# Performance work log

Measured on AMD Instinct MI355X. Metric: run time of the kernel, lower is better.

The kernel has to match this reference:

```python
import jax, jax.numpy as jnp
import numpy as np

B, S, TK, H, E, V, OOV = 16, 8, 400, 256, 128, 50000, 50
H2 = 2 * H


def setup_inputs() -> dict:
    key = jax.random.key(0)
    ks = jax.random.split(key, 24)
    std = 0.02
    d = {}
    d["y_t_1"] = jax.random.randint(ks[0], (B,), 0, V)
    d["h0"] = jax.random.normal(ks[1], (B, H), jnp.float32)
    d["c0"] = jax.random.normal(ks[2], (B, H), jnp.float32)
    d["encoder_output"] = jax.random.normal(ks[3], (B, S, TK, H2), jnp.float32)
    d["section_output"] = jax.random.normal(ks[4], (B, S, H2), jnp.float32)
    d["enc_padding_mask"] = jnp.ones((B, S, TK), jnp.float32)
    d["c_t_1"] = jax.random.normal(ks[5], (B, H2), jnp.float32)
    d["extra_zeros"] = jnp.zeros((B, OOV), jnp.float32)
    d["enc_batch_extend_vocab"] = jax.random.randint(ks[6], (B, S * TK), 0, V + OOV)
    d["coverage"] = jnp.zeros((B, S, TK), jnp.float32)
    d["gamma"] = jnp.ones((B, S, TK), jnp.float32)
    # learned parameters
    d["embedding"] = std * jax.random.normal(ks[7], (V, E), jnp.float32)
    d["W_xc"] = std * jax.random.normal(ks[8], (H2 + E, E), jnp.float32)
    d["b_xc"] = jnp.zeros((E,), jnp.float32)
    d["W_ih"] = std * jax.random.normal(ks[9], (E, 4 * H), jnp.float32)
    d["b_ih"] = jnp.zeros((4 * H,), jnp.float32)
    d["W_hh"] = std * jax.random.normal(ks[10], (H, 4 * H), jnp.float32)
    # pytorch init sets forget-gate bias (2nd quarter) to 1
    d["b_hh"] = jnp.zeros((4 * H,), jnp.float32).at[H:2 * H].set(1.0)
    d["Wh_sec"] = std * jax.random.normal(ks[11], (H2, H2), jnp.float32)
    d["Wd_sec"] = std * jax.random.normal(ks[12], (H2, H2), jnp.float32)
    d["bd_sec"] = jnp.zeros((H2,), jnp.float32)
    d["v_sec"] = std * jax.random.normal(ks[13], (H2, 1), jnp.float32)
    d["Wh_w"] = std * jax.random.normal(ks[14], (H2, H2), jnp.float32)
    d["Wc_w"] = std * jax.random.normal(ks[15], (H2,), jnp.float32)
    d["Wd_w"] = std * jax.random.normal(ks[16], (H2, H2), jnp.float32)
    d["bd_w"] = jnp.zeros((H2,), jnp.float32)
    d["v_w"] = std * jax.random.normal(ks[17], (H2, 1), jnp.float32)
    d["W_pgen"] = std * jax.random.normal(ks[18], (4 * H + E, 1), jnp.float32)
    d["b_pgen"] = jnp.zeros((1,), jnp.float32)
    d["W_out1"] = std * jax.random.normal(ks[19], (3 * H, H), jnp.float32)
    d["b_out1"] = jnp.zeros((H,), jnp.float32)
    d["W_out2"] = std * jax.random.normal(ks[20], (H, V), jnp.float32)
    d["b_out2"] = jnp.zeros((V,), jnp.float32)
    return d


def reference(y_t_1, h0, c0, encoder_output, section_output, enc_padding_mask,
              c_t_1, extra_zeros, enc_batch_extend_vocab, coverage, gamma,
              embedding, W_xc, b_xc, W_ih, b_ih, W_hh, b_hh,
              Wh_sec, Wd_sec, bd_sec, v_sec,
              Wh_w, Wc_w, Wd_w, bd_w, v_w,
              W_pgen, b_pgen, W_out1, b_out1, W_out2, b_out2):
    # embedding + input context projection
    emb = embedding[y_t_1]                                      # [B,E]
    x = jnp.concatenate([c_t_1, emb], axis=1) @ W_xc + b_xc     # [B,E]
    # single-step LSTM (pytorch gate order i,f,g,o)
    gates = x @ W_ih + b_ih + h0 @ W_hh + b_hh                  # [B,4H]
    i, f, g, o = jnp.split(gates, 4, axis=1)
    c = jax.nn.sigmoid(f) * c0 + jax.nn.sigmoid(i) * jnp.tanh(g)
    h = jax.nn.sigmoid(o) * jnp.tanh(c)
    s_t_hat = jnp.concatenate([h, c], axis=1)                   # [B,2H]
    # section attention -> beta [B,S]
    e_sec = jnp.tanh(section_output @ Wh_sec + (s_t_hat @ Wd_sec + bd_sec)[:, None, :])
    sc_sec = jnp.squeeze(e_sec @ v_sec, -1)                     # [B,S]
    beta = jax.nn.softmax(sc_sec, axis=1)
    beta = beta / beta.sum(axis=1, keepdims=True)
    # word attention with coverage feature
    att = encoder_output @ Wh_w + (s_t_hat @ Wd_w + bd_w)[:, None, None, :]
    att = att + coverage[..., None] * Wc_w                      # [B,S,TK,2H]
    sc_w = jnp.squeeze(jnp.tanh(att) @ v_w, -1)                 # [B,S,TK]
    ws = (beta[:, :, None] * sc_w).reshape(B, S * TK)
    mask = enc_padding_mask.reshape(B, S * TK)
    ad = jax.nn.softmax(ws, axis=1) * mask
    attn = ad / ad.sum(axis=1, keepdims=True)                   # [B,S*TK]
    c_t = jnp.einsum('bt,btn->bn', attn, encoder_output.reshape(B, S * TK, H2))
    cov = coverage + attn.reshape(B, S, TK)
    # pointer-gen gate
    p_gen = jax.nn.sigmoid(jnp.concatenate([c_t, s_t_hat, x], axis=1) @ W_pgen + b_pgen)  # [B,1]
    # output vocab distribution
    out = jnp.concatenate([h, c_t], axis=1) @ W_out1 + b_out1
    vocab_dist = jax.nn.softmax(out @ W_out2 + b_out2, axis=1)  # [B,V]
    vd = jnp.concatenate([p_gen * vocab_dist, extra_zeros], axis=1)  # [B,V+OOV]
    ad_ = (1.0 - p_gen) * attn
    rows = jnp.arange(B)[:, None]
    final_dist = vd.at[rows, enc_batch_extend_vocab].add(ad_)
    return (final_dist, h, c, c_t, attn, p_gen, cov)
```

## Files before the change

kernel.cpp:

```cpp
#include <hip/hip_runtime.h>
#include <math.h>

#define BB   16
#define SS   8
#define TKK  400
#define HH   256
#define EE   128
#define VV   50000
#define OOVV 50
#define HH2  512
#define STK  (SS*TKK)
#define VOO  (VV+OOVV)

#define OFF_X     0
#define OFF_ST    2048
#define OFF_SD    10240
#define OFF_WD    18432
#define OFF_SCSEC 26752
#define OFF_SCW   26880
#define OFF_CT    78080
#define OFF_OUT1  86272
#define OFF_PGEN  90368
#define OFF_PSUM  93520
#define OFF_ASUM  99776
#define OFF_BT    113040

#define O_FD   0
#define O_H    800800
#define O_C    804896
#define O_CT   808992
#define O_ATTN 817184
#define O_PGEN 868384
#define O_COV  868400

#define NLB 391
#define GEMM_NB 800

typedef __attribute__((ext_vector_type(8))) short bf16x8;
typedef __attribute__((ext_vector_type(4))) float f32x4;

__device__ __forceinline__ float sigm(float x){ return 1.0f/(1.0f+expf(-x)); }

__device__ __forceinline__ unsigned short f2b(float f){
  unsigned int u = __float_as_uint(f);
  unsigned int r = (u + 0x7fffu + ((u >> 16) & 1u)) >> 16;
  return (unsigned short)r;
}

__device__ __forceinline__ float tanhfast(float x){
  float cx = fminf(9.0f, fmaxf(-9.0f, x));
  float t = __expf(2.0f*cx);
  return (t - 1.0f) * __builtin_amdgcn_rcpf(t + 1.0f);
}

__device__ __forceinline__ float wave_sum(float v){
  #pragma unroll
  for(int o=32;o>0;o>>=1) v += __shfl_xor(v,o);
  return v;
}

__device__ __forceinline__ void glds16(const void* g, void* l){
  __builtin_amdgcn_global_load_lds((const __attribute__((address_space(1))) void*)g,
                                   (__attribute__((address_space(3))) void*)l, 16, 0, 0);
}

__device__ __forceinline__ bf16x8 cvt8(float4 a, float4 b){
  union{ bf16x8 v; unsigned short u[8]; } t;
  t.u[0]=f2b(a.x); t.u[1]=f2b(a.y); t.u[2]=f2b(a.z); t.u[3]=f2b(a.w);
  t.u[4]=f2b(b.x); t.u[5]=f2b(b.y); t.u[6]=f2b(b.z); t.u[7]=f2b(b.w);
  return t.v;
}

__global__ void k_pre(const float* __restrict__ Whw, unsigned short* __restrict__ Btg,
                      const int* __restrict__ y, const float* __restrict__ ct1,
                      const float* __restrict__ emb, const float* __restrict__ Wxc,
                      const float* __restrict__ bxc, const float* __restrict__ bdsec,
                      const float* __restrict__ bdw, float* __restrict__ ws){
  __shared__ float sm[10440];
  int bi = blockIdx.x, tid = threadIdx.x;
  if(bi < 64){
    int n0 = (bi & 7)*64, k0 = (bi >> 3)*64;
    int tx = tid & 63, ty = tid >> 6;
    #pragma unroll
    for(int it=0; it<16; it++){
      int kk = it*4 + ty;
      sm[kk*65 + tx] = Whw[(size_t)(k0+kk)*HH2 + n0 + tx];
    }
    __syncthreads();
    #pragma unroll
    for(int it=0; it<2; it++){
      int kgl = it*4 + ty;
      int kgG = (k0 >> 3) + kgl;
      int rnd = kgG >> 2, kg = kgG & 3;
      int col = n0 + tx;
      union{ bf16x8 v; unsigned short u[8]; } t;
      #pragma unroll
      for(int j=0;j<8;j++) t.u[j] = f2b(sm[(kgl*8+j)*65 + tx]);
      *(bf16x8*)&Btg[(size_t)rnd*16384 + (size_t)(col*4 + (kg ^ ((col>>1)&3)))*8] = t.v;
    }
  } else if(bi < 80){
    float* cat = sm;
    float* red = sm + 10240;
    for(int f=tid; f<BB*640; f+=256){
      int b = f/640, r = f - b*640;
      cat[f] = (r < HH2) ? ct1[b*HH2 + r] : emb[(size_t)y[b]*EE + (r-HH2)];
    }
    __syncthreads();
    int c = (bi-64)*8 + (tid & 7);
    int b = (tid >> 3) & 15;
    int kh = tid >> 7;
    float acc = 0.0f;
    const float* a = &cat[b*640];
    for(int k=kh*320; k<kh*320+320; k++) acc += a[k]*Wxc[k*EE + c];
    if(kh==1) red[b*8 + (tid&7)] = acc;
    __syncthreads();
    if(kh==0) ws[OFF_X + b*EE + c] = acc + red[b*8 + (tid&7)] + bxc[c];
  } else {
    for(int f=tid; f<BB*HH2; f+=256){
      int c = f & (HH2-1);
      ws[OFF_CT + f] = 0.0f;
      ws[OFF_SD + f] = bdsec[c];
      ws[OFF_WD + f] = bdw[c];
    }
    if(tid < BB) ws[OFF_ASUM + tid] = 0.0f;
  }
}

__global__ void k_lstm(const float* __restrict__ h0, const float* __restrict__ c0,
                       const float* __restrict__ Wih, const float* __restrict__ bih,
                       const float* __restrict__ Whh, const float* __restrict__ bhh,
                       float* __restrict__ ws, float* __restrict__ out){
  __shared__ float xh[4*384];
  __shared__ float red[3*64*4];
  int tid = threadIdx.x;
  int jc = (blockIdx.x & 15)*16, bc = (blockIdx.x >> 4)*4;
  for(int f=tid; f<4*384; f+=256){
    int bl = f/384, r = f - bl*384;
    xh[f] = (r < EE) ? ws[OFF_X + (bc+bl)*EE + r] : h0[(bc+bl)*HH + (r-EE)];
  }
  __syncthreads();
  int jl = tid & 15, bl = (tid >> 4) & 3, kq = tid >> 6;
  int j = jc + jl, b = bc + bl;
  float a0=0.f, a1=0.f, a2=0.f, a3=0.f;
  const float* a = &xh[bl*384];
  for(int k=kq*96; k<kq*96+96; k++){
    float v = a[k];
    const float* w = (k < EE) ? &Wih[k*4*HH + j] : &Whh[(k-EE)*4*HH + j];
    a0 += v*w[0]; a1 += v*w[HH]; a2 += v*w[2*HH]; a3 += v*w[3*HH];
  }
  if(kq){
    float* r = &red[((kq-1)*64 + bl*16 + jl)*4];
    r[0]=a0; r[1]=a1; r[2]=a2; r[3]=a3;
  }
  __syncthreads();
  if(kq==0){
    #pragma unroll
    for(int p=0;p<3;p++){
      const float* r = &red[(p*64 + bl*16 + jl)*4];
      a0+=r[0]; a1+=r[1]; a2+=r[2]; a3+=r[3];
    }
    a0 += bih[j] + bhh[j];
    a1 += bih[j+HH] + bhh[j+HH];
    a2 += bih[j+2*HH] + bhh[j+2*HH];
    a3 += bih[j+3*HH] + bhh[j+3*HH];
    float c = sigm(a1)*c0[b*HH+j] + sigm(a0)*tanhf(a2);
    float h = sigm(a3)*tanhf(c);
    out[O_H + b*HH + j] = h;
    out[O_C + b*HH + j] = c;
    ws[OFF_ST + b*HH2 + j]      = h;
    ws[OFF_ST + b*HH2 + HH + j] = c;
  }
}

__global__ void k_proj(const float* __restrict__ Wdsec, const float* __restrict__ Wdw,
                       float* __restrict__ ws){
  __shared__ float st[BB*32];
  int tid = threadIdx.x;
  int mi = blockIdx.x >> 5;
  int cb = (blockIdx.x >> 4) & 1;
  int kq = blockIdx.x & 15;
  int k0 = kq*32;
  for(int f=tid; f<BB*32; f+=256){
    int b = f >> 5, kk = f & 31;
    st[f] = ws[OFF_ST + b*HH2 + k0 + kk];
  }
  __syncthreads();
  int c = cb*256 + tid;
  const float* Wm = (mi ? Wdw : Wdsec) + (size_t)k0*HH2 + c;
  float acc[BB];
  #pragma unroll
  for(int b=0;b<BB;b++) acc[b] = 0.0f;
  #pragma unroll 4
  for(int kk=0;kk<32;kk++){
    float wv = Wm[(size_t)kk*HH2];
    #pragma unroll
    for(int b=0;b<BB;b++) acc[b] += st[b*32 + kk]*wv;
  }
  int dst = mi ? OFF_WD : OFF_SD;
  #pragma unroll
  for(int b=0;b<BB;b++) atomicAdd(&ws[dst + b*HH2 + c], acc[b]);
}

__global__ __launch_bounds__(512, 4) void k_gemm6(
        const float* __restrict__ A, const unsigned short* __restrict__ Btg,
        const float* __restrict__ Wcw, const float* __restrict__ vw,
        const float* __restrict__ cover,
        const float* __restrict__ sec, const float* __restrict__ Whsec,
        const float* __restrict__ vsec, float* __restrict__ ws){
  __shared__ __align__(16) unsigned short smem[32768];
  int tid = threadIdx.x;
  if(blockIdx.x >= GEMM_NB){
    float* row = (float*)smem;
    float* red = row + HH2;
    int bi = blockIdx.x - GEMM_NB;
    int b = bi >> 3;
    if(tid < HH2) row[tid] = sec[(size_t)bi*HH2 + tid];
    __syncthreads();
    int col = tid;
    float acc = 0.0f;
    #pragma unroll 8
    for(int k=0;k<HH2;k++) acc += row[k]*Whsec[k*HH2 + col];
    float val = tanhf(acc + ws[OFF_SD + b*HH2 + col]) * vsec[col];
    val = wave_sum(val);
    if((tid&63)==0) red[tid>>6] = val;
    __syncthreads();
    if(tid==0){
      float s = 0.0f;
      #pragma unroll
      for(int i=0;i<8;i++) s += red[i];
      ws[OFF_SCSEC + bi] = s;
    }
    return;
  }
  int w = tid >> 6, lane = tid & 63, m = lane & 15, q = lane >> 4;
  int mk = (m >> 1) & 3, sw = q ^ mk;
  int rg = w >> 1, cg = w & 1;
  int row0 = blockIdx.x * 64;
  int b = blockIdx.x / 50;

  const float* arow_p = &A[(size_t)(row0 + rg*16 + m)*HH2 + q*8];

  f32x4 acc[16];
  #pragma unroll
  for(int j=0;j<16;j++) acc[j] = (f32x4){0.f,0.f,0.f,0.f};

  #define GLDSB(rr, bufsel) {                                                  \
    const unsigned short* bsrc_ = Btg + (size_t)(rr)*16384;                    \
    _Pragma("unroll")                                                          \
    for(int i_=0;i_<4;i_++)                                                    \
      glds16(bsrc_ + i_*4096 + tid*8, &smem[(bufsel)*16384 + i_*4096 + tid*8]);\
  }

  GLDSB(0, 0);
  float4 pa0 = *(const float4*)(arow_p);
  float4 pa1 = *(const float4*)(arow_p + 4);
  GLDSB(1, 1);
  asm volatile("s_waitcnt vmcnt(6)" ::: "memory");
  __builtin_amdgcn_sched_barrier(0);
  bf16x8 af = cvt8(pa0, pa1);
  __builtin_amdgcn_s_barrier();

  #pragma unroll
  for(int r=0; r<16; r++){
    if(r < 15){
      pa0 = *(const float4*)(arow_p + (r+1)*32);
      pa1 = *(const float4*)(arow_p + (r+1)*32 + 4);
    }
    __builtin_amdgcn_s_setprio(1);
    #pragma unroll
    for(int cf=0; cf<16; cf++){
      int col = cg*256 + cf*16 + m;
      bf16x8 bv = *(const bf16x8*)&smem[(size_t)(r&1)*16384 + ((size_t)col*4 + sw)*8];
      acc[cf] = __builtin_amdgcn_mfma_f32_16x16x32_bf16(af, bv, acc[cf], 0,0,0);
    }
    __builtin_amdgcn_s_setprio(0);
    if(r < 14){
      asm volatile("s_waitcnt lgkmcnt(0)" ::: "memory");
      __builtin_amdgcn_sched_barrier(0);
      __builtin_amdgcn_s_barrier();
      GLDSB(r+2, (r&1));
    }
    if(r < 15){
      if(r < 14){ asm volatile("s_waitcnt vmcnt(6)" ::: "memory"); }
      else      { asm volatile("s_waitcnt vmcnt(2)" ::: "memory"); }
      __builtin_amdgcn_sched_barrier(0);
      af = cvt8(pa0, pa1);
      __builtin_amdgcn_s_barrier();
    }
  }
  #undef GLDSB

  float cov[4];
  #pragma unroll
  for(int r=0;r<4;r++) cov[r] = cover[row0 + rg*16 + q*4 + r];
  float rsum[4] = {0,0,0,0};
  #pragma unroll
  for(int j=0;j<16;j++){
    int col = cg*256 + j*16 + m;
    float wdv = ws[OFF_WD + b*HH2 + col];
    float wcv = Wcw[col], vwv = vw[col];
    #pragma unroll
    for(int r=0;r<4;r++)
      rsum[r] += tanhfast(acc[j][r] + wdv + cov[r]*wcv) * vwv;
  }
  __syncthreads();
  float* rbuf = (float*)smem;
  #pragma unroll
  for(int r=0;r<4;r++){
    float v = rsum[r];
    v += __shfl_xor(v,1,16); v += __shfl_xor(v,2,16);
    v += __shfl_xor(v,4,16); v += __shfl_xor(v,8,16);
    if(m==0) rbuf[cg*64 + rg*16 + q*4 + r] = v;
  }
  __syncthreads();
  if(tid < 64) ws[OFF_SCW + row0 + tid] = rbuf[tid] + rbuf[64 + tid];
}

__global__ void k_attnA(const float* __restrict__ mask, float* __restrict__ ws,
                        float* __restrict__ out){
  int b = blockIdx.y;
  int j = blockIdx.x*256 + threadIdx.x;
  float sc[SS];
  #pragma unroll
  for(int s=0;s<SS;s++) sc[s] = ws[OFF_SCSEC + b*SS + s];
  float bm = -1e30f;
  #pragma unroll
  for(int s=0;s<SS;s++) bm = fmaxf(bm, sc[s]);
  float bsum = 0.0f;
  #pragma unroll
  for(int s=0;s<SS;s++){ sc[s] = expf(sc[s]-bm); bsum += sc[s]; }
  float e = 0.0f;
  if(j < STK){
    float be = sc[j/TKK] / bsum;
    e = expf(be * ws[OFF_SCW + b*STK + j]) * mask[b*STK + j];
    out[O_ATTN + b*STK + j] = e;
  }
  float sv = wave_sum(e);
  if((threadIdx.x & 63) == 0) atomicAdd(&ws[OFF_ASUM + b], sv);
}

__global__ void k_attnB(const float* __restrict__ enc, const float* __restrict__ cover,
                        float* __restrict__ ws, float* __restrict__ out){
  int b = blockIdx.y, tid = threadIdx.x;
  __shared__ float a[64];
  __shared__ float part[512];
  int t0 = blockIdx.x*64;
  float inv = 1.0f / ws[OFF_ASUM + b];
  if(tid < 64){
    float av = out[O_ATTN + b*STK + t0 + tid] * inv;
    a[tid] = av;
    out[O_ATTN + b*STK + t0 + tid] = av;
    out[O_COV  + b*STK + t0 + tid] = cover[b*STK + t0 + tid] + av;
  }
  __syncthreads();
  int c4 = tid & 127, rh = tid >> 7;
  const float4* e4 = (const float4*)enc;
  size_t base = ((size_t)(b*STK + t0 + rh*32))*128 + c4;
  float4 acc = {0.f,0.f,0.f,0.f};
  #pragma unroll 8
  for(int rr=0; rr<32; rr++){
    float4 v = e4[base + (size_t)rr*128];
    float av = a[rh*32 + rr];
    acc.x += av*v.x; acc.y += av*v.y; acc.z += av*v.z; acc.w += av*v.w;
  }
  if(rh) *(float4*)&part[c4*4] = acc;
  __syncthreads();
  if(!rh){
    float4 o = *(const float4*)&part[c4*4];
    atomicAdd(&ws[OFF_CT + b*HH2 + c4*4 + 0], acc.x + o.x);
    atomicAdd(&ws[OFF_CT + b*HH2 + c4*4 + 1], acc.y + o.y);
    atomicAdd(&ws[OFF_CT + b*HH2 + c4*4 + 2], acc.z + o.z);
    atomicAdd(&ws[OFF_CT + b*HH2 + c4*4 + 3], acc.w + o.w);
  }
}

__global__ void k_out1(const float* __restrict__ Wp, const float* __restrict__ bp,
                       const float* __restrict__ Wo1, const float* __restrict__ bo1,
                       float* __restrict__ ws, float* __restrict__ out){
  __shared__ float cat[BB*768];
  __shared__ float red[3*64];
  int tid = threadIdx.x;
  if(blockIdx.x == 64){
    int w = tid >> 6, lane = tid & 63;
    #pragma unroll
    for(int i=0;i<4;i++){
      int b = w*4 + i;
      float p = 0.0f;
      for(int k=lane;k<4*HH+EE;k+=64){
        float val = (k < HH2) ? ws[OFF_CT + b*HH2 + k]
                  : (k < 4*HH) ? ws[OFF_ST + b*HH2 + (k-HH2)]
                  : ws[OFF_X + b*EE + (k-4*HH)];
        p += val * Wp[k];
      }
      p = wave_sum(p);
      if(lane==0){
        float pg = sigm(p + bp[0]);
        ws[OFF_PGEN + b] = pg;
        out[O_PGEN + b]  = pg;
      }
    }
    for(int f=tid; f<BB*HH2; f+=256) out[O_CT + f] = ws[OFF_CT + f];
    return;
  }
  for(int f=tid; f<BB*768; f+=256){
    int b = f/768, r = f - b*768;
    cat[f] = (r < HH) ? ws[OFF_ST + b*HH2 + r] : ws[OFF_CT + b*HH2 + (r-HH)];
  }
  __syncthreads();
  int cl = tid & 3, bl = (tid >> 2) & 15, kq = tid >> 6;
  int c = blockIdx.x*4 + cl;
  float acc = 0.0f;
  const float* a = &cat[bl*768];
  for(int k=kq*192; k<kq*192+192; k++) acc += a[k]*Wo1[k*HH + c];
  if(kq) red[(kq-1)*64 + bl*4 + cl] = acc;
  __syncthreads();
  if(kq==0){
    acc += red[bl*4+cl] + red[64 + bl*4+cl] + red[128 + bl*4+cl];
    ws[OFF_OUT1 + bl*HH + c] = acc + bo1[c];
  }
}

__global__ void k_logits(const float* __restrict__ W2, const float* __restrict__ b2,
                         float* __restrict__ ws, float* __restrict__ out){
  int tid = threadIdx.x;
  __shared__ float o1[BB*HH];
  for(int i=tid;i<BB*HH/4;i+=256)
    ((float4*)o1)[i] = ((const float4*)&ws[OFF_OUT1])[i];
  __syncthreads();
  int cl = tid & 31, bq = tid >> 5;
  int c4 = blockIdx.x*128 + cl*4;
  bool ok = c4 < VV;
  int b0 = bq*2, b1 = b0+1;
  float4 acc0 = {0.f,0.f,0.f,0.f}, acc1 = {0.f,0.f,0.f,0.f};
  if(ok){
    const float* oa = &o1[b0*HH];
    const float* ob = &o1[b1*HH];
    #pragma unroll 4
    for(int k=0;k<HH;k++){
      float4 wv = *(const float4*)&W2[(size_t)k*VV + c4];
      float xa = oa[k], xb = ob[k];
      acc0.x += xa*wv.x; acc0.y += xa*wv.y; acc0.z += xa*wv.z; acc0.w += xa*wv.w;
      acc1.x += xb*wv.x; acc1.y += xb*wv.y; acc1.z += xb*wv.z; acc1.w += xb*wv.w;
    }
  }
  float bv[4] = {0,0,0,0};
  if(ok){ float4 t = *(const float4*)&b2[c4]; bv[0]=t.x; bv[1]=t.y; bv[2]=t.z; bv[3]=t.w; }
  float a0[4] = {acc0.x, acc0.y, acc0.z, acc0.w};
  float a1[4] = {acc1.x, acc1.y, acc1.z, acc1.w};
  float s0 = 0.0f, s1 = 0.0f;
  #pragma unroll
  for(int j=0;j<4;j++){
    float e0 = ok ? expf(a0[j]+bv[j]) : 0.0f;
    float e1 = ok ? expf(a1[j]+bv[j]) : 0.0f;
    if(ok){
      out[(size_t)b0*VOO + c4 + j] = e0;
      out[(size_t)b1*VOO + c4 + j] = e1;
    }
    s0 += e0; s1 += e1;
  }
  #pragma unroll
  for(int o=1;o<32;o<<=1){ s0 += __shfl_xor(s0,o,32); s1 += __shfl_xor(s1,o,32); }
  if(cl==0){
    ws[OFF_PSUM + b0*NLB + blockIdx.x] = s0;
    ws[OFF_PSUM + b1*NLB + blockIdx.x] = s1;
  }
}

__global__ void k_final(const float* __restrict__ xz, float* __restrict__ ws,
                        float* __restrict__ out){
  int b = blockIdx.y;
  int v = blockIdx.x*256 + threadIdx.x;
  __shared__ float red[4];
  int lane = threadIdx.x & 63, w = threadIdx.x >> 6;
  float p = 0.0f;
  for(int i=threadIdx.x;i<NLB;i+=256) p += ws[OFF_PSUM + b*NLB + i];
  p = wave_sum(p);
  if(lane==0) red[w] = p;
  __syncthreads();
  float s = red[0]+red[1]+red[2]+red[3];
  float pg = ws[OFF_PGEN + b];
  if(v < VV)       out[(size_t)b*VOO + v] = pg * out[(size_t)b*VOO + v] / s;
  else if(v < VOO) out[(size_t)b*VOO + v] = xz[b*OOVV + (v-VV)];
}

__global__ void k_scatter(const int* __restrict__ ebev, float* __restrict__ ws,
                          float* __restrict__ out){
  int b = blockIdx.y;
  float r = 1.0f - ws[OFF_PGEN + b];
  for(int j=blockIdx.x*256+threadIdx.x;j<STK;j+=1024){
    int idx = ebev[b*STK + j];
    atomicAdd(&out[(size_t)b*VOO + idx], r*out[O_ATTN + b*STK + j]);
  }
}

extern "C" void kernel_launch(void* const* d_in, const int* in_sizes, int n_in,
                              void* d_out, int out_size, void* d_ws, size_t ws_size,
                              hipStream_t stream){
  const int*   y     = (const int*)  d_in[0];
  const float* h0    = (const float*)d_in[1];
  const float* c0    = (const float*)d_in[2];
  const float* enc   = (const float*)d_in[3];
  const float* sec   = (const float*)d_in[4];
  const float* mask  = (const float*)d_in[5];
  const float* ct1   = (const float*)d_in[6];
  const float* xz    = (const float*)d_in[7];
  const int*   ebev  = (const int*)  d_in[8];
  const float* cover = (const float*)d_in[9];
  const float* emb   = (const float*)d_in[11];
  const float* Wxc   = (const float*)d_in[12];
  const float* bxc   = (const float*)d_in[13];
  const float* Wih   = (const float*)d_in[14];
  const float* bih   = (const float*)d_in[15];
  const float* Whh   = (const float*)d_in[16];
  const float* bhh   = (const float*)d_in[17];
  const float* Whsec = (const float*)d_in[18];
  const float* Wdsec = (const float*)d_in[19];
  const float* bdsec = (const float*)d_in[20];
  const float* vsec  = (const float*)d_in[21];
  const float* Whw   = (const float*)d_in[22];
  const float* Wcw   = (const float*)d_in[23];
  const float* Wdw   = (const float*)d_in[24];
  const float* bdw   = (const float*)d_in[25];
  const float* vw    = (const float*)d_in[26];
  const float* Wp    = (const float*)d_in[27];
  const float* bp    = (const float*)d_in[28];
  const float* Wo1   = (const float*)d_in[29];
  const float* bo1   = (const float*)d_in[30];
  const float* Wo2   = (const float*)d_in[31];
  const float* bo2   = (const float*)d_in[32];
  float* out = (float*)d_out;
  float* ws  = (float*)d_ws;
  unsigned short* Btg = (unsigned short*)(ws + OFF_BT);

  k_pre    <<<dim3(81),       dim3(256),  0, stream>>>(Whw, Btg, y, ct1, emb, Wxc, bxc, bdsec, bdw, ws);
  k_lstm   <<<dim3(64),       dim3(256),  0, stream>>>(h0, c0, Wih, bih, Whh, bhh, ws, out);
  k_proj   <<<dim3(64),       dim3(256),  0, stream>>>(Wdsec, Wdw, ws);
  k_gemm6  <<<dim3(928),      dim3(512),  0, stream>>>(enc, Btg, Wcw, vw, cover, sec, Whsec, vsec, ws);
  k_attnA  <<<dim3(13,BB),    dim3(256),  0, stream>>>(mask, ws, out);
  k_attnB  <<<dim3(50,BB),    dim3(256),  0, stream>>>(enc, cover, ws, out);
  k_out1   <<<dim3(65),       dim3(256),  0, stream>>>(Wp, bp, Wo1, bo1, ws, out);
  k_logits <<<dim3(NLB),      dim3(256),  0, stream>>>(Wo2, bo2, ws, out);
  k_final  <<<dim3(196,BB),   dim3(256),  0, stream>>>(xz, ws, out);
  k_scatter<<<dim3(4,BB),     dim3(256),  0, stream>>>(ebev, ws, out);
}
```

Before: 466.2 us.

## Fuse attention, output projection, logits and scatter into one cooperative kernel

Replaces six separate tail kernels (attention softmax, context vector, out1/pgen, logits, final normalization, scatter) with a single cooperative-groups kernel on 512 blocks that uses grid-wide syncs between phases. The aim is to remove per-launch overhead and the gaps between small kernels. In exchange, each phase is limited to the fixed grid size, and grid syncs carry their own cost. The out1 phase now reads its inputs straight from global memory instead of staging them in shared memory, and the vocab-sum reduction becomes a separate phase.

```diff
diff --git a/kernel.cpp b/kernel.cpp
--- a/kernel.cpp
+++ b/kernel.cpp
@@ -1,5 +1,8 @@
 #include <hip/hip_runtime.h>
+#include <hip/hip_cooperative_groups.h>
 #include <math.h>
+
+namespace cg = cooperative_groups;
 
 #define BB   16
 #define SS   8
@@ -23,6 +26,7 @@
 #define OFF_PGEN  90368
 #define OFF_PSUM  93520
 #define OFF_ASUM  99776
+#define OFF_VSUM  99792
 #define OFF_BT    113040
 
 #define O_FD   0
@@ -35,6 +39,7 @@
 
 #define NLB 391
 #define GEMM_NB 800
+#define TAILB 512
 
 typedef __attribute__((ext_vector_type(8))) short bf16x8;
 typedef __attribute__((ext_vector_type(4))) float f32x4;
@@ -316,180 +321,188 @@
   if(tid < 64) ws[OFF_SCW + row0 + tid] = rbuf[tid] + rbuf[64 + tid];
 }
 
-__global__ void k_attnA(const float* __restrict__ mask, float* __restrict__ ws,
-                        float* __restrict__ out){
-  int b = blockIdx.y;
-  int j = blockIdx.x*256 + threadIdx.x;
-  float sc[SS];
-  #pragma unroll
-  for(int s=0;s<SS;s++) sc[s] = ws[OFF_SCSEC + b*SS + s];
-  float bm = -1e30f;
-  #pragma unroll
-  for(int s=0;s<SS;s++) bm = fmaxf(bm, sc[s]);
-  float bsum = 0.0f;
-  #pragma unroll
-  for(int s=0;s<SS;s++){ sc[s] = expf(sc[s]-bm); bsum += sc[s]; }
-  float e = 0.0f;
-  if(j < STK){
-    float be = sc[j/TKK] / bsum;
-    e = expf(be * ws[OFF_SCW + b*STK + j]) * mask[b*STK + j];
-    out[O_ATTN + b*STK + j] = e;
-  }
-  float sv = wave_sum(e);
-  if((threadIdx.x & 63) == 0) atomicAdd(&ws[OFF_ASUM + b], sv);
-}
-
-__global__ void k_attnB(const float* __restrict__ enc, const float* __restrict__ cover,
-                        float* __restrict__ ws, float* __restrict__ out){
-  int b = blockIdx.y, tid = threadIdx.x;
-  __shared__ float a[64];
-  __shared__ float part[512];
-  int t0 = blockIdx.x*64;
-  float inv = 1.0f / ws[OFF_ASUM + b];
-  if(tid < 64){
-    float av = out[O_ATTN + b*STK + t0 + tid] * inv;
-    a[tid] = av;
-    out[O_ATTN + b*STK + t0 + tid] = av;
-    out[O_COV  + b*STK + t0 + tid] = cover[b*STK + t0 + tid] + av;
-  }
-  __syncthreads();
-  int c4 = tid & 127, rh = tid >> 7;
-  const float4* e4 = (const float4*)enc;
-  size_t base = ((size_t)(b*STK + t0 + rh*32))*128 + c4;
-  float4 acc = {0.f,0.f,0.f,0.f};
-  #pragma unroll 8
-  for(int rr=0; rr<32; rr++){
-    float4 v = e4[base + (size_t)rr*128];
-    float av = a[rh*32 + rr];
-    acc.x += av*v.x; acc.y += av*v.y; acc.z += av*v.z; acc.w += av*v.w;
-  }
-  if(rh) *(float4*)&part[c4*4] = acc;
-  __syncthreads();
-  if(!rh){
-    float4 o = *(const float4*)&part[c4*4];
-    atomicAdd(&ws[OFF_CT + b*HH2 + c4*4 + 0], acc.x + o.x);
-    atomicAdd(&ws[OFF_CT + b*HH2 + c4*4 + 1], acc.y + o.y);
-    atomicAdd(&ws[OFF_CT + b*HH2 + c4*4 + 2], acc.z + o.z);
-    atomicAdd(&ws[OFF_CT + b*HH2 + c4*4 + 3], acc.w + o.w);
-  }
-}
-
-__global__ void k_out1(const float* __restrict__ Wp, const float* __restrict__ bp,
-                       const float* __restrict__ Wo1, const float* __restrict__ bo1,
-                       float* __restrict__ ws, float* __restrict__ out){
-  __shared__ float cat[BB*768];
-  __shared__ float red[3*64];
-  int tid = threadIdx.x;
-  if(blockIdx.x == 64){
-    int w = tid >> 6, lane = tid & 63;
-    #pragma unroll
-    for(int i=0;i<4;i++){
-      int b = w*4 + i;
-      float p = 0.0f;
-      for(int k=lane;k<4*HH+EE;k+=64){
-        float val = (k < HH2) ? ws[OFF_CT + b*HH2 + k]
-                  : (k < 4*HH) ? ws[OFF_ST + b*HH2 + (k-HH2)]
-                  : ws[OFF_X + b*EE + (k-4*HH)];
-        p += val * Wp[k];
+__global__ __launch_bounds__(256, 2) void k_tail(
+        const float* __restrict__ enc, const float* __restrict__ cover,
+        const float* __restrict__ mask,
+        const float* __restrict__ Wp,  const float* __restrict__ bp,
+        const float* __restrict__ Wo1, const float* __restrict__ bo1,
+        const float* __restrict__ W2,  const float* __restrict__ b2,
+        const float* __restrict__ xz,  const int* __restrict__ ebev,
+        float* __restrict__ ws, float* __restrict__ out){
+  cg::grid_group gg = cg::this_grid();
+  __shared__ __align__(16) float sm[4160];
+  int tid = threadIdx.x, bid = blockIdx.x;
+
+  {
+    int idx = bid*256 + tid;
+    float e = 0.0f; int b = 0;
+    if(idx < BB*STK){
+      b = idx / STK;
+      float sc[SS];
+      #pragma unroll
+      for(int s=0;s<SS;s++) sc[s] = ws[OFF_SCSEC + b*SS + s];
+      float bm = -1e30f;
+      #pragma unroll
+      for(int s=0;s<SS;s++) bm = fmaxf(bm, sc[s]);
+      float bsum = 0.0f;
+      #pragma unroll
+      for(int s=0;s<SS;s++){ sc[s] = expf(sc[s]-bm); bsum += sc[s]; }
+      float be = sc[(idx - b*STK)/TKK] / bsum;
+      e = expf(be * ws[OFF_SCW + idx]) * mask[idx];
+      out[O_ATTN + idx] = e;
+    }
+    float sv = wave_sum(e);
+    if((tid & 63) == 0 && idx < BB*STK) atomicAdd(&ws[OFF_ASUM + b], sv);
+  }
+  gg.sync();
+
+  for(int vt = bid; vt < 800; vt += TAILB){
+    float* a = sm;
+    float* part = sm + 64;
+    int b = vt / 50, t0 = (vt - b*50)*64;
+    float inv = 1.0f / ws[OFF_ASUM + b];
+    if(tid < 64){
+      float av = out[O_ATTN + b*STK + t0 + tid] * inv;
+      a[tid] = av;
+      out[O_ATTN + b*STK + t0 + tid] = av;
+      out[O_COV  + b*STK + t0 + tid] = cover[b*STK + t0 + tid] + av;
+    }
+    __syncthreads();
+    int c4 = tid & 127, rh = tid >> 7;
+    const float4* e4 = (const float4*)enc;
+    size_t base = ((size_t)(b*STK + t0 + rh*32))*128 + c4;
+    float4 acc = {0.f,0.f,0.f,0.f};
+    #pragma unroll 8
+    for(int rr=0; rr<32; rr++){
+      float4 v = e4[base + (size_t)rr*128];
+      float av = a[rh*32 + rr];
+      acc.x += av*v.x; acc.y += av*v.y; acc.z += av*v.z; acc.w += av*v.w;
+    }
+    if(rh) *(float4*)&part[c4*4] = acc;
+    __syncthreads();
+    if(!rh){
+      float4 o = *(const float4*)&part[c4*4];
+      atomicAdd(&ws[OFF_CT + b*HH2 + c4*4 + 0], acc.x + o.x);
+      atomicAdd(&ws[OFF_CT + b*HH2 + c4*4 + 1], acc.y + o.y);
+      atomicAdd(&ws[OFF_CT + b*HH2 + c4*4 + 2], acc.z + o.z);
+      atomicAdd(&ws[OFF_CT + b*HH2 + c4*4 + 3], acc.w + o.w);
+    }
+    __syncthreads();
+  }
+  gg.sync();
+
+  if(bid < 65){
+    if(bid == 64){
+      int w = tid >> 6, lane = tid & 63;
+      #pragma unroll
+      for(int i=0;i<4;i++){
+        int b = w*4 + i;
+        float p = 0.0f;
+        for(int k=lane;k<4*HH+EE;k+=64){
+          float val = (k < HH2) ? ws[OFF_CT + b*HH2 + k]
+                    : (k < 4*HH) ? ws[OFF_ST + b*HH2 + (k-HH2)]
+                    : ws[OFF_X + b*EE + (k-4*HH)];
+          p += val * Wp[k];
+        }
+        p = wave_sum(p);
+        if(lane==0){
+          float pg = sigm(p + bp[0]);
+          ws[OFF_PGEN + b] = pg;
+          out[O_PGEN + b]  = pg;
+        }
       }
-      p = wave_sum(p);
-      if(lane==0){
-        float pg = sigm(p + bp[0]);
-        ws[OFF_PGEN + b] = pg;
-        out[O_PGEN + b]  = pg;
+      for(int f=tid; f<BB*HH2; f+=256) out[O_CT + f] = ws[OFF_CT + f];
+    } else {
+      float* red = sm;
+      int cl = tid & 3, bl = (tid >> 2) & 15, kq = tid >> 6;
+      int c = bid*4 + cl;
+      float acc = 0.0f;
+      for(int k=kq*192; k<kq*192+192; k++){
+        float val = (k < HH) ? ws[OFF_ST + bl*HH2 + k] : ws[OFF_CT + bl*HH2 + (k-HH)];
+        acc += val * Wo1[k*HH + c];
       }
-    }
-    for(int f=tid; f<BB*HH2; f+=256) out[O_CT + f] = ws[OFF_CT + f];
-    return;
-  }
-  for(int f=tid; f<BB*768; f+=256){
-    int b = f/768, r = f - b*768;
-    cat[f] = (r < HH) ? ws[OFF_ST + b*HH2 + r] : ws[OFF_CT + b*HH2 + (r-HH)];
-  }
-  __syncthreads();
-  int cl = tid & 3, bl = (tid >> 2) & 15, kq = tid >> 6;
-  int c = blockIdx.x*4 + cl;
-  float acc = 0.0f;
-  const float* a = &cat[bl*768];
-  for(int k=kq*192; k<kq*192+192; k++) acc += a[k]*Wo1[k*HH + c];
-  if(kq) red[(kq-1)*64 + bl*4 + cl] = acc;
-  __syncthreads();
-  if(kq==0){
-    acc += red[bl*4+cl] + red[64 + bl*4+cl] + red[128 + bl*4+cl];
-    ws[OFF_OUT1 + bl*HH + c] = acc + bo1[c];
-  }
-}
-
-__global__ void k_logits(const float* __restrict__ W2, const float* __restrict__ b2,
-                         float* __restrict__ ws, float* __restrict__ out){
-  int tid = threadIdx.x;
-  __shared__ float o1[BB*HH];
-  for(int i=tid;i<BB*HH/4;i+=256)
-    ((float4*)o1)[i] = ((const float4*)&ws[OFF_OUT1])[i];
-  __syncthreads();
-  int cl = tid & 31, bq = tid >> 5;
-  int c4 = blockIdx.x*128 + cl*4;
-  bool ok = c4 < VV;
-  int b0 = bq*2, b1 = b0+1;
-  float4 acc0 = {0.f,0.f,0.f,0.f}, acc1 = {0.f,0.f,0.f,0.f};
-  if(ok){
-    const float* oa = &o1[b0*HH];
-    const float* ob = &o1[b1*HH];
-    #pragma unroll 4
-    for(int k=0;k<HH;k++){
-      float4 wv = *(const float4*)&W2[(size_t)k*VV + c4];
-      float xa = oa[k], xb = ob[k];
-      acc0.x += xa*wv.x; acc0.y += xa*wv.y; acc0.z += xa*wv.z; acc0.w += xa*wv.w;
-      acc1.x += xb*wv.x; acc1.y += xb*wv.y; acc1.z += xb*wv.z; acc1.w += xb*wv.w;
-    }
-  }
-  float bv[4] = {0,0,0,0};
-  if(ok){ float4 t = *(const float4*)&b2[c4]; bv[0]=t.x; bv[1]=t.y; bv[2]=t.z; bv[3]=t.w; }
-  float a0[4] = {acc0.x, acc0.y, acc0.z, acc0.w};
-  float a1[4] = {acc1.x, acc1.y, acc1.z, acc1.w};
-  float s0 = 0.0f, s1 = 0.0f;
-  #pragma unroll
-  for(int j=0;j<4;j++){
-    float e0 = ok ? expf(a0[j]+bv[j]) : 0.0f;
-    float e1 = ok ? expf(a1[j]+bv[j]) : 0.0f;
+      if(kq) red[(kq-1)*64 + bl*4 + cl] = acc;
+      __syncthreads();
+      if(kq==0){
+        acc += red[bl*4+cl] + red[64 + bl*4+cl] + red[128 + bl*4+cl];
+        ws[OFF_OUT1 + bl*HH + c] = acc + bo1[c];
+      }
+    }
+  }
+  gg.sync();
+
+  if(bid < NLB){
+    float* o1 = sm;
+    for(int i=tid;i<BB*HH/4;i+=256)
+      ((float4*)o1)[i] = ((const float4*)&ws[OFF_OUT1])[i];
+    __syncthreads();
+    int cl = tid & 31, bq = tid >> 5;
+    int c4 = bid*128 + cl*4;
+    bool ok = c4 < VV;
+    int b0 = bq*2, b1 = b0+1;
+    float4 acc0 = {0.f,0.f,0.f,0.f}, acc1 = {0.f,0.f,0.f,0.f};
     if(ok){
-      out[(size_t)b0*VOO + c4 + j] = e0;
-      out[(size_t)b1*VOO + c4 + j] = e1;
-    }
-    s0 += e0; s1 += e1;
-  }
-  #pragma unroll
-  for(int o=1;o<32;o<<=1){ s0 += __shfl_xor(s0,o,32); s1 += __shfl_xor(s1,o,32); }
-  if(cl==0){
-    ws[OFF_PSUM + b0*NLB + blockIdx.x] = s0;
-    ws[OFF_PSUM + b1*NLB + blockIdx.x] = s1;
-  }
-}
-
-__global__ void k_final(const float* __restrict__ xz, float* __restrict__ ws,
-                        float* __restrict__ out){
-  int b = blockIdx.y;
-  int v = blockIdx.x*256 + threadIdx.x;
-  __shared__ float red[4];
-  int lane = threadIdx.x & 63, w = threadIdx.x >> 6;
-  float p = 0.0f;
-  for(int i=threadIdx.x;i<NLB;i+=256) p += ws[OFF_PSUM + b*NLB + i];
-  p = wave_sum(p);
-  if(lane==0) red[w] = p;
-  __syncthreads();
-  float s = red[0]+red[1]+red[2]+red[3];
-  float pg = ws[OFF_PGEN + b];
-  if(v < VV)       out[(size_t)b*VOO + v] = pg * out[(size_t)b*VOO + v] / s;
-  else if(v < VOO) out[(size_t)b*VOO + v] = xz[b*OOVV + (v-VV)];
-}
-
-__global__ void k_scatter(const int* __restrict__ ebev, float* __restrict__ ws,
-                          float* __restrict__ out){
-  int b = blockIdx.y;
-  float r = 1.0f - ws[OFF_PGEN + b];
-  for(int j=blockIdx.x*256+threadIdx.x;j<STK;j+=1024){
-    int idx = ebev[b*STK + j];
-    atomicAdd(&out[(size_t)b*VOO + idx], r*out[O_ATTN + b*STK + j]);
+      const float* oa = &o1[b0*HH];
+      const float* ob = &o1[b1*HH];
+      #pragma unroll 4
+      for(int k=0;k<HH;k++){
+        float4 wv = *(const float4*)&W2[(size_t)k*VV + c4];
+        float xa = oa[k], xb = ob[k];
+        acc0.x += xa*wv.x; acc0.y += xa*wv.y; acc0.z += xa*wv.z; acc0.w += xa*wv.w;
+        acc1.x += xb*wv.x; acc1.y += xb*wv.y; acc1.z += xb*wv.z; acc1.w += xb*wv.w;
+      }
+    }
+    float bv[4] = {0,0,0,0};
+    if(ok){ float4 t = *(const float4*)&b2[c4]; bv[0]=t.x; bv[1]=t.y; bv[2]=t.z; bv[3]=t.w; }
+    float a0[4] = {acc0.x, acc0.y, acc0.z, acc0.w};
+    float a1[4] = {acc1.x, acc1.y, acc1.z, acc1.w};
+    float s0 = 0.0f, s1 = 0.0f;
+    #pragma unroll
+    for(int j=0;j<4;j++){
+      float e0 = ok ? expf(a0[j]+bv[j]) : 0.0f;
+      float e1 = ok ? expf(a1[j]+bv[j]) : 0.0f;
+      if(ok){
+        out[(size_t)b0*VOO + c4 + j] = e0;
+        out[(size_t)b1*VOO + c4 + j] = e1;
+      }
+      s0 += e0; s1 += e1;
+    }
+    #pragma unroll
+    for(int o=1;o<32;o<<=1){ s0 += __shfl_xor(s0,o,32); s1 += __shfl_xor(s1,o,32); }
+    if(cl==0){
+      ws[OFF_PSUM + b0*NLB + bid] = s0;
+      ws[OFF_PSUM + b1*NLB + bid] = s1;
+    }
+  }
+  gg.sync();
+
+  if(bid < BB){
+    float* red = sm;
+    float p = 0.0f;
+    for(int i=tid;i<NLB;i+=256) p += ws[OFF_PSUM + bid*NLB + i];
+    p = wave_sum(p);
+    if((tid&63)==0) red[tid>>6] = p;
+    __syncthreads();
+    if(tid==0) ws[OFF_VSUM + bid] = red[0]+red[1]+red[2]+red[3];
+  }
+  gg.sync();
+
+  for(int idx = bid*256 + tid; idx < BB*VOO; idx += TAILB*256){
+    int b = idx / VOO;
+    int v = idx - b*VOO;
+    float pg = ws[OFF_PGEN + b];
+    if(v < VV) out[idx] = pg * out[idx] / ws[OFF_VSUM + b];
+    else       out[idx] = xz[b*OOVV + (v-VV)];
+  }
+  gg.sync();
+
+  {
+    int idx = bid*256 + tid;
+    if(idx < BB*STK){
+      int b = idx / STK;
+      float r = 1.0f - ws[OFF_PGEN + b];
+      atomicAdd(&out[(size_t)b*VOO + ebev[idx]], r*out[O_ATTN + idx]);
+    }
   }
 }
 
@@ -536,10 +549,11 @@
   k_lstm   <<<dim3(64),       dim3(256),  0, stream>>>(h0, c0, Wih, bih, Whh, bhh, ws, out);
   k_proj   <<<dim3(64),       dim3(256),  0, stream>>>(Wdsec, Wdw, ws);
   k_gemm6  <<<dim3(928),      dim3(512),  0, stream>>>(enc, Btg, Wcw, vw, cover, sec, Whsec, vsec, ws);
-  k_attnA  <<<dim3(13,BB),    dim3(256),  0, stream>>>(mask, ws, out);
-  k_attnB  <<<dim3(50,BB),    dim3(256),  0, stream>>>(enc, cover, ws, out);
-  k_out1   <<<dim3(65),       dim3(256),  0, stream>>>(Wp, bp, Wo1, bo1, ws, out);
-  k_logits <<<dim3(NLB),      dim3(256),  0, stream>>>(Wo2, bo2, ws, out);
-  k_final  <<<dim3(196,BB),   dim3(256),  0, stream>>>(xz, ws, out);
-  k_scatter<<<dim3(4,BB),     dim3(256),  0, stream>>>(ebev, ws, out);
-}
+
+  void* targs[] = {(void*)&enc, (void*)&cover, (void*)&mask,
+                   (void*)&Wp, (void*)&bp, (void*)&Wo1, (void*)&bo1,
+                   (void*)&Wo2, (void*)&bo2, (void*)&xz, (void*)&ebev,
+                   (void*)&ws, (void*)&out};
+  hipLaunchCooperativeKernel((const void*)k_tail, dim3(TAILB), dim3(256),
+                             targs, 0, stream);
+}
```

After: 835.8 us. +79.3%, slower.
